# Optimization experiments

Measured on AMD Instinct MI355X. Metric: run time of the kernel, lower is better.

The kernel has to match this reference:

```python
import jax, jax.numpy as jnp
from jax import lax
import numpy as np

B, P, N = 4, 12000, 100   # batch, max_pillars, max_points_per_pillar
H, W = 108, 124           # pseudo-image size from forward()
DN = ('NCHW', 'HWIO', 'NCHW')


def _conv(x, k, b):
    y = lax.conv_general_dilated(x, k, (1, 1), 'SAME', dimension_numbers=DN)
    return y + b[None, :, None, None]


def _cbr(x, k, b, s, t):
    # Conv2d + folded BatchNorm2d (eval: per-channel scale/shift) + ReLU
    y = _conv(x, k, b)
    return jax.nn.relu(y * s[None, :, None, None] + t[None, :, None, None])


def _pool(x):
    return lax.reduce_window(x, -jnp.inf, lax.max, (1, 1, 2, 2), (1, 1, 2, 2), 'VALID')


def setup_inputs() -> dict:
    key = jax.random.key(0)
    ks = iter(jax.random.split(key, 64))
    d = {}
    d['pillars'] = jax.random.normal(next(ks), (B, P, N, 9), jnp.float32)

    def w(shape, scale=0.05):
        return jax.random.normal(next(ks), shape, jnp.float32) * scale

    d['w1'] = w((9, 64)); d['b1'] = w((64,))
    d['s1'] = 1.0 + w((64,)); d['t1'] = w((64,))
    d['w2'] = w((64, 64)); d['b2'] = w((64,))
    d['s2'] = 1.0 + w((64,)); d['t2'] = w((64,))
    chans = [(64, 64), (64, 64), (64, 128), (128, 128), (128, 256), (256, 256)]
    for i, (ci, co) in enumerate(chans, 1):
        d['ck%d' % i] = w((3, 3, ci, co)); d['cb%d' % i] = w((co,))
        d['cs%d' % i] = 1.0 + w((co,)); d['ct%d' % i] = w((co,))
    d['hk1'] = w((3, 3, 256, 256)); d['hb1'] = w((256,))
    d['hk2'] = w((1, 1, 256, 10)); d['hb2'] = w((10,))
    d['num_points'] = jax.random.randint(next(ks), (B, P), 0, 100, jnp.int32)
    return d


def reference(pillars, w1, b1, s1, t1, w2, b2, s2, t2,
              ck1, cb1, cs1, ct1, ck2, cb2, cs2, ct2,
              ck3, cb3, cs3, ct3, ck4, cb4, cs4, ct4,
              ck5, cb5, cs5, ct5, ck6, cb6, cs6, ct6,
              hk1, hb1, hk2, hb2, num_points):
    # pillar feature net: Linear+BN(folded)+ReLU x2, batched over all points  [B,P,N,9] -> [B,P,N,64]
    h = jax.nn.relu((pillars @ w1 + b1) * s1 + t1)
    h = jax.nn.relu((h @ w2 + b2) * s2 + t2)
    # masked segment-max over the variable-length point groups
    mask = jnp.arange(N)[None, None, :] < num_points[:, :, None]          # [B,P,N]
    neg = jnp.finfo(h.dtype).min
    feat = jnp.max(jnp.where(mask[..., None], h, neg), axis=2)            # [B,P,64]
    valid = num_points > 0
    feat = jnp.where(valid[..., None], feat, 0.0)
    cnt = jnp.maximum(jnp.sum(valid, axis=1), 1).astype(feat.dtype)       # [B]
    mean = jnp.sum(feat, axis=1) / cnt[:, None]                           # [B,64]
    # nearest-interpolate a 1x1 map to HxW == broadcast
    x = jnp.broadcast_to(mean[:, :, None, None], (pillars.shape[0], 64, H, W))
    # 2D backbone
    x = _cbr(x, ck1, cb1, cs1, ct1); x = _cbr(x, ck2, cb2, cs2, ct2); x = _pool(x)
    x = _cbr(x, ck3, cb3, cs3, ct3); x = _cbr(x, ck4, cb4, cs4, ct4); x = _pool(x)
    x = _cbr(x, ck5, cb5, cs5, ct5); x = _cbr(x, ck6, cb6, cs6, ct6)
    # detection head
    y = jax.nn.relu(_conv(x, hk1, hb1))
    return _conv(y, hk2, hb2)   # [B, num_classes+7=10, 27, 31]
```

## Files before the change

kernel.cpp:

```cpp
#include <hip/hip_runtime.h>

typedef __bf16 vbf8 __attribute__((ext_vector_type(8)));
typedef __bf16 vbf4 __attribute__((ext_vector_type(4)));
typedef unsigned short us8 __attribute__((ext_vector_type(8)));
typedef float f32x4 __attribute__((ext_vector_type(4)));
typedef float f32x4u __attribute__((ext_vector_type(4), aligned(4)));

#define NBLK 64

__device__ __forceinline__ int caseof(int h, int H, int e) {
  if (h < 0 || h >= H) return -1;
  if (h < e) return h;
  if (h >= H - e) return h - (H - 1) + 2 * e;
  return e;
}
__device__ __forceinline__ int repof(int i, int H, int eo) {
  return (i <= eo) ? i : H - 1 - 2 * eo + i;
}

__device__ __forceinline__ void gridbar(int* bar) {
  __syncthreads();
  if (threadIdx.x == 0) {
    int* cnt = bar; int* gen = bar + 1;
    int g = __hip_atomic_load(gen, __ATOMIC_RELAXED, __HIP_MEMORY_SCOPE_AGENT);
    if (__hip_atomic_fetch_add(cnt, 1, __ATOMIC_ACQ_REL, __HIP_MEMORY_SCOPE_AGENT) == NBLK - 1) {
      __hip_atomic_store(cnt, 0, __ATOMIC_RELAXED, __HIP_MEMORY_SCOPE_AGENT);
      __hip_atomic_store(gen, g + 1, __ATOMIC_RELEASE, __HIP_MEMORY_SCOPE_AGENT);
    } else {
      while (__hip_atomic_load(gen, __ATOMIC_RELAXED, __HIP_MEMORY_SCOPE_AGENT) == g)
        __builtin_amdgcn_s_sleep(8);
      __threadfence();
    }
  }
  __syncthreads();
}

__global__ void setup_kernel(const float* __restrict__ w1, const float* __restrict__ b1,
                             const float* __restrict__ s1, const float* __restrict__ t1,
                             const float* __restrict__ w2, const float* __restrict__ b2,
                             const float* __restrict__ s2, const float* __restrict__ t2,
                             __bf16* __restrict__ wfrag, float* __restrict__ be2f) {
  int l = threadIdx.x;
  int s = l & 15, g = l >> 4;
#pragma unroll
  for (int m = 0; m < 4; ++m) {
    int c = 32 * (m & 1) + 8 * (s >> 2) + 4 * (m >> 1) + (s & 3);
#pragma unroll
    for (int e = 0; e < 8; ++e) {
      int k = g * 8 + e;
      float v = 0.f;
      if (k < 9)       v = w1[k * 64 + c] * s1[c];
      else if (k == 9) v = fmaf(b1[c], s1[c], t1[c]);
      wfrag[(m * 64 + l) * 8 + e] = (__bf16)v;
    }
    int co = s + 16 * m;
#pragma unroll
    for (int e = 0; e < 8; ++e) {
      int k = g * 8 + e;
      wfrag[((4 + m) * 64 + l) * 8 + e] = (__bf16)(w2[k * 64 + co] * s2[co]);
      wfrag[((8 + m) * 64 + l) * 8 + e] = (__bf16)(w2[(32 + k) * 64 + co] * s2[co]);
    }
    be2f[m * 64 + l] = fmaf(b2[co], s2[co], t2[co]);
  }
}

__global__ __launch_bounds__(256) void convw_kernel(
    const float* __restrict__ k1, const float* __restrict__ k2,
    const float* __restrict__ k3, const float* __restrict__ k4,
    const float* __restrict__ k5, const float* __restrict__ k6,
    const float* __restrict__ kh, __bf16* __restrict__ wT) {
  __shared__ float tile[64][65];
  const int tCI[7]    = {64, 64, 64, 128, 128, 256, 256};
  const int tCO[7]    = {64, 64, 128, 128, 256, 256, 256};
  const int tOFF[7]   = {0, 36864, 73728, 147456, 294912, 589824, 1179648};
  const int tTILES[7] = {9, 9, 18, 36, 72, 144, 144};
  int bid = blockIdx.x;
  int ti = 0, acc = 0;
  while (ti < 6 && bid >= acc + tTILES[ti]) { acc += tTILES[ti]; ++ti; }
  int lt = bid - acc;
  int CI = tCI[ti], CO = tCO[ti];
  const float* src;
  if (ti == 0) src = k1; else if (ti == 1) src = k2; else if (ti == 2) src = k3;
  else if (ti == 3) src = k4; else if (ti == 4) src = k5; else if (ti == 5) src = k6;
  else src = kh;
  int cot = CO / 64, tpt = (CI / 64) * cot;
  int tap = lt / tpt; int r2 = lt - tap * tpt;
  int ci0 = (r2 / cot) * 64, co0 = (r2 % cot) * 64;
  const float* sp = src + (size_t)(tap * CI + ci0) * CO + co0;
  int t = threadIdx.x;
  int lr = t >> 6, lc = t & 63;
#pragma unroll
  for (int rr = 0; rr < 64; rr += 4)
    tile[rr + lr][lc] = sp[(size_t)(rr + lr) * CO + lc];
  __syncthreads();
  __bf16* dst = wT + tOFF[ti] + ((size_t)tap * CO + co0) * CI + ci0;
#pragma unroll
  for (int rr = 0; rr < 64; rr += 4)
    dst[(size_t)(rr + lr) * CI + lc] = (__bf16)tile[lc][rr + lr];
}

__global__ __launch_bounds__(256) void pillar_kernel(
    const float* __restrict__ pil, const int* __restrict__ npt,
    const __bf16* __restrict__ wfrag, const float* __restrict__ be2f,
    float* __restrict__ partial, int* __restrict__ pcnt)
{
  __shared__ float redf[4][64];
  __shared__ int redc[4];
  const int tid = threadIdx.x;
  const int wv = tid >> 6, lane = tid & 63;
  const int s = lane & 15, g = lane >> 4;
  const int wid = blockIdx.x * 4 + wv;
  const int b = wid / 6000;
  const int p0 = (wid - b * 6000) * 2;

  vbf8 w1f[4], w2f0[4], w2f1[4];
  float be2[4];
#pragma unroll
  for (int m = 0; m < 4; ++m) {
    w1f[m]  = *(const vbf8*)(wfrag + ((0 + m) * 64 + lane) * 8);
    w2f0[m] = *(const vbf8*)(wfrag + ((4 + m) * 64 + lane) * 8);
    w2f1[m] = *(const vbf8*)(wfrag + ((8 + m) * 64 + lane) * 8);
    be2[m] = be2f[m * 64 + lane];
  }

  float fsum[4] = {0.f, 0.f, 0.f, 0.f};
  int cnt = 0;

  for (int i = 0; i < 2; ++i) {
    int pidx = b * 12000 + p0 + i;
    int np = npt[pidx];
    if (np <= 0) continue;
    ++cnt;
    float feat[4][4];
#pragma unroll
    for (int n = 0; n < 4; ++n)
#pragma unroll
      for (int r = 0; r < 4; ++r) feat[n][r] = 0.f;

    int ngrp = (np + 15) >> 4;
    const float* pbase = pil + (size_t)pidx * 900;
    const float* pp0 = pbase + s * 9;
    f32x4u lo = *(const f32x4u*)pp0;
    f32x4u hi = *(const f32x4u*)(pp0 + 4);
    float v8 = pp0[8];
    for (int grp = 0; grp < ngrp; ++grp) {
      int g2 = min(grp + 1, ngrp - 1);
      int ptn = min(g2 * 16 + s, 99);
      const float* ppn = pbase + ptn * 9;
      f32x4u nlo = *(const f32x4u*)ppn;
      f32x4u nhi = *(const f32x4u*)(ppn + 4);
      float nv8 = ppn[8];

      vbf8 b1f;
      b1f[0] = (__bf16)(g == 0 ? lo[0] : (g == 1 ? v8 : 0.f));
      b1f[1] = (__bf16)(g == 0 ? lo[1] : (g == 1 ? 1.0f : 0.f));
      b1f[2] = (__bf16)(g == 0 ? lo[2] : 0.f);
      b1f[3] = (__bf16)(g == 0 ? lo[3] : 0.f);
      b1f[4] = (__bf16)(g == 0 ? hi[0] : 0.f);
      b1f[5] = (__bf16)(g == 0 ? hi[1] : 0.f);
      b1f[6] = (__bf16)(g == 0 ? hi[2] : 0.f);
      b1f[7] = (__bf16)(g == 0 ? hi[3] : 0.f);

      const f32x4 z = {0.f, 0.f, 0.f, 0.f};
      f32x4 d1[4];
#pragma unroll
      for (int m = 0; m < 4; ++m)
        d1[m] = __builtin_amdgcn_mfma_f32_16x16x32_bf16(w1f[m], b1f, z, 0, 0, 0);

      vbf8 a2f0, a2f1;
#pragma unroll
      for (int r = 0; r < 4; ++r) {
        a2f0[r]     = (__bf16)fmaxf(d1[0][r], 0.f);
        a2f1[r]     = (__bf16)fmaxf(d1[1][r], 0.f);
        a2f0[4 + r] = (__bf16)fmaxf(d1[2][r], 0.f);
        a2f1[4 + r] = (__bf16)fmaxf(d1[3][r], 0.f);
      }

      f32x4 d2[4];
#pragma unroll
      for (int n = 0; n < 4; ++n) {
        f32x4 cb = {be2[n], be2[n], be2[n], be2[n]};
        d2[n] = __builtin_amdgcn_mfma_f32_16x16x32_bf16(a2f0, w2f0[n], cb, 0, 0, 0);
        d2[n] = __builtin_amdgcn_mfma_f32_16x16x32_bf16(a2f1, w2f1[n], d2[n], 0, 0, 0);
      }
      if (((grp + 1) << 4) <= np) {
#pragma unroll
        for (int n = 0; n < 4; ++n)
#pragma unroll
          for (int r = 0; r < 4; ++r) feat[n][r] = fmaxf(feat[n][r], d2[n][r]);
      } else {
#pragma unroll
        for (int n = 0; n < 4; ++n)
#pragma unroll
          for (int r = 0; r < 4; ++r) {
            float vv = (grp * 16 + 4 * g + r < np) ? d2[n][r] : 0.f;
            feat[n][r] = fmaxf(feat[n][r], vv);
          }
      }
      lo = nlo; hi = nhi; v8 = nv8;
    }
#pragma unroll
    for (int n = 0; n < 4; ++n) {
      float m = fmaxf(fmaxf(feat[n][0], feat[n][1]), fmaxf(feat[n][2], feat[n][3]));
      m = fmaxf(m, __shfl_xor(m, 16));
      m = fmaxf(m, __shfl_xor(m, 32));
      fsum[n] += m;
    }
  }
  if (g == 0) {
#pragma unroll
    for (int n = 0; n < 4; ++n) redf[wv][s + 16 * n] = fsum[n];
  }
  if (lane == 0) redc[wv] = cnt;
  __syncthreads();
  if (tid < 64) {
    float tot = redf[0][tid] + redf[1][tid] + redf[2][tid] + redf[3][tid];
    partial[blockIdx.x * 64 + tid] = tot;
    if (tid == 0) pcnt[blockIdx.x] = redc[0] + redc[1] + redc[2] + redc[3];
  }
}

__global__ void mean_kernel(const float* __restrict__ partial,
                            const int* __restrict__ pcnt,
                            __bf16* __restrict__ x0,
                            __bf16* __restrict__ zbuf, int* __restrict__ bar) {
  int b = blockIdx.x, t = threadIdx.x;
  if (b == 0) {
    zbuf[t] = (__bf16)0.f;
    if (t < 2) bar[t] = 0;
  }
  int c = t & 63, q = t >> 6;
  float sum = 0.f;
  for (int w = q; w < 1500; w += 4) sum += partial[(b * 1500 + w) * 64 + c];
  int cl = 0;
  for (int w = t; w < 1500; w += 256) cl += pcnt[b * 1500 + w];
  __shared__ float sh[256];
  __shared__ int shc[256];
  sh[t] = sum; shc[t] = cl;
  __syncthreads();
  for (int o = 128; o > 0; o >>= 1) {
    if (t < o) shc[t] += shc[t + o];
    __syncthreads();
  }
  if (t < 64) {
    float tot = sh[t] + sh[t + 64] + sh[t + 128] + sh[t + 192];
    x0[b * 64 + t] = (__bf16)(tot / (float)(shc[0] > 0 ? shc[0] : 1));
  }
}

template <int CI, int CO, int H, int EIN, bool HAS_BN, bool OUT_F32>
__device__ __forceinline__ void caseconv_dev(
    int wid, const __bf16* __restrict__ xin, const __bf16* __restrict__ wt,
    const float* __restrict__ cb, const float* __restrict__ cs,
    const float* __restrict__ ct, __bf16* __restrict__ yout,
    float* __restrict__ yf32, const __bf16* __restrict__ zbuf)
{
  constexpr int EOUT = EIN + 1;
  constexpr int NBI = 2 * EIN + 1;
  constexpr int NBO = 2 * EOUT + 1;
  constexpr int M = NBO * NBO * 4;
  constexpr int NT = CO / 16;
  constexpr int KC = CI / 32;
  constexpr int MT = (M + 31) / 32;
  if (wid >= MT * NT) return;
  const int lane = threadIdx.x & 63;
  const int s = lane & 15, g = lane >> 4;
  const int nt = wid % NT, mt = wid / NT;

  const __bf16* pa[2][9];
#pragma unroll
  for (int mf = 0; mf < 2; ++mf) {
    int m = mt * 32 + mf * 16 + s; if (m >= M) m = M - 1;
    int b = m & 3, q = m >> 2;
    int bw = q % NBO, bh = q / NBO;
    int reph = repof(bh, H, EOUT), repw = repof(bw, H, EOUT);
#pragma unroll
    for (int dh = 0; dh < 3; ++dh)
#pragma unroll
      for (int dw = 0; dw < 3; ++dw) {
        int jh = caseof(reph + dh - 1, H, EIN);
        int jw = caseof(repw + dw - 1, H, EIN);
        bool v = (jh >= 0) && (jw >= 0);
        pa[mf][dh * 3 + dw] =
            v ? xin + (size_t)((jh * NBI + jw) * 4 + b) * CI : zbuf;
      }
  }

  f32x4 acc0 = {0.f, 0.f, 0.f, 0.f}, acc1 = {0.f, 0.f, 0.f, 0.f};
#pragma unroll
  for (int tap = 0; tap < 9; ++tap) {
    const __bf16* wtap = wt + ((size_t)tap * CO + nt * 16) * CI + 8 * g;
#pragma unroll
    for (int ck = 0; ck < KC; ++ck) {
      vbf8 a0 = *(const vbf8*)(pa[0][tap] + ck * 32 + 8 * g);
      vbf8 a1 = *(const vbf8*)(pa[1][tap] + ck * 32 + 8 * g);
      vbf8 bb = *(const vbf8*)(wtap + (size_t)s * CI + ck * 32);
      acc0 = __builtin_amdgcn_mfma_f32_16x16x32_bf16(a0, bb, acc0, 0, 0, 0);
      acc1 = __builtin_amdgcn_mfma_f32_16x16x32_bf16(a1, bb, acc1, 0, 0, 0);
    }
  }

  int co = nt * 16 + s;
  float sc, sh;
  if (HAS_BN) { sc = cs[co]; sh = fmaf(cb[co], sc, ct[co]); }
  else        { sc = 1.f;    sh = cb[co]; }
#pragma unroll
  for (int mf = 0; mf < 2; ++mf) {
    f32x4 acc = mf ? acc1 : acc0;
#pragma unroll
    for (int r = 0; r < 4; ++r) {
      int m = mt * 32 + mf * 16 + 4 * g + r;
      if (m < M) {
        float v = fmaxf(fmaf(acc[r], sc, sh), 0.f);
        if constexpr (OUT_F32) yf32[(size_t)m * CO + co] = v;
        else                   yout[(size_t)m * CO + co] = (__bf16)v;
      }
    }
  }
}

template <int C, int HOUT, int EIN>
__device__ __forceinline__ void casepool_dev(int gtid, const __bf16* __restrict__ xin,
                                             __bf16* __restrict__ yout) {
  constexpr int EOUT = (EIN + 1) / 2;
  constexpr int NBI = 2 * EIN + 1;
  constexpr int NBO = 2 * EOUT + 1;
  constexpr int C8 = C / 8;
  for (int idx = gtid; idx < NBO * NBO * 4 * C8; idx += NBLK * 256) {
    int c8 = idx % C8; int rest = idx / C8;
    int b = rest & 3; int pos = rest >> 2;
    int iw = pos % NBO, ih = pos / NBO;
    int rh = repof(ih, HOUT, EOUT), rw = repof(iw, HOUT, EOUT);
    int h0 = caseof(2 * rh, 2 * HOUT, EIN), h1 = caseof(2 * rh + 1, 2 * HOUT, EIN);
    int w0 = caseof(2 * rw, 2 * HOUT, EIN), w1 = caseof(2 * rw + 1, 2 * HOUT, EIN);
    const unsigned short* xp = (const unsigned short*)xin;
    us8 v00 = *(const us8*)(xp + (size_t)((h0 * NBI + w0) * 4 + b) * C + c8 * 8);
    us8 v01 = *(const us8*)(xp + (size_t)((h0 * NBI + w1) * 4 + b) * C + c8 * 8);
    us8 v10 = *(const us8*)(xp + (size_t)((h1 * NBI + w0) * 4 + b) * C + c8 * 8);
    us8 v11 = *(const us8*)(xp + (size_t)((h1 * NBI + w1) * 4 + b) * C + c8 * 8);
    us8 o;
#pragma unroll
    for (int e = 0; e < 8; ++e) {
      unsigned short a = v00[e] > v01[e] ? v00[e] : v01[e];
      unsigned short c = v10[e] > v11[e] ? v10[e] : v11[e];
      o[e] = a > c ? a : c;
    }
    *(us8*)((unsigned short*)yout + (size_t)((ih * NBO + iw) * 4 + b) * C + c8 * 8) = o;
  }
}

__device__ __forceinline__ void head2c_dev(int gtid, const float* __restrict__ x,
                                           const float* __restrict__ wk,
                                           const float* __restrict__ bias,
                                           float* __restrict__ y) {
  for (int idx = gtid; idx < 121 * 4 * 16; idx += NBLK * 256) {
    int co = idx & 15;
    if (co >= 10) continue;
    int q = idx >> 4;
    const float* xr = x + (size_t)q * 256;
    float acc = 0.f;
#pragma unroll 4
    for (int ci = 0; ci < 256; ci += 4) {
      float4 in4 = *(const float4*)(xr + ci);
      acc = fmaf(in4.x, wk[(ci + 0) * 10 + co], acc);
      acc = fmaf(in4.y, wk[(ci + 1) * 10 + co], acc);
      acc = fmaf(in4.z, wk[(ci + 2) * 10 + co], acc);
      acc = fmaf(in4.w, wk[(ci + 3) * 10 + co], acc);
    }
    y[(size_t)q * 10 + co] = acc + bias[co];
  }
}

__device__ __forceinline__ void scatter_dev(int gtid, const float* __restrict__ y,
                                            float* __restrict__ out) {
  for (int idx = gtid; idx < 4 * 10 * 27 * 31; idx += NBLK * 256) {
    int c = idx % 31;
    int r = (idx / 31) % 27;
    int ch = (idx / (31 * 27)) % 10;
    int b = idx / (31 * 27 * 10);
    int rr = (r <= 7) ? r : ((r >= 20) ? r - 11 : 7);
    int cc = (c <= 7) ? c : ((c >= 24) ? c - 15 : 7);
    int ph = caseof(rr, 16, 5), pw = caseof(cc, 16, 5);
    out[idx] = y[(size_t)(((ph * 11 + pw) * 4 + b)) * 10 + ch];
  }
}

__global__ __launch_bounds__(256) void backbone_kernel(
    const __bf16* __restrict__ X0, __bf16* __restrict__ X1, __bf16* __restrict__ X2,
    __bf16* __restrict__ P1, __bf16* __restrict__ X3, __bf16* __restrict__ X4,
    __bf16* __restrict__ P2, __bf16* __restrict__ X5, __bf16* __restrict__ X6,
    float* __restrict__ XH, float* __restrict__ h2out,
    const __bf16* wt1, const __bf16* wt2, const __bf16* wt3, const __bf16* wt4,
    const __bf16* wt5, const __bf16* wt6, const __bf16* wth,
    const float* cb1, const float* cs1, const float* ct1,
    const float* cb2, const float* cs2, const float* ct2,
    const float* cb3, const float* cs3, const float* ct3,
    const float* cb4, const float* cs4, const float* ct4,
    const float* cb5, const float* cs5, const float* ct5,
    const float* cb6, const float* cs6, const float* ct6,
    const float* hb1, const float* hk2, const float* hb2,
    const __bf16* __restrict__ zbuf, int* __restrict__ bar, float* __restrict__ out)
{
  const int wid = blockIdx.x * 4 + (threadIdx.x >> 6);
  const int gtid = blockIdx.x * 256 + threadIdx.x;

  caseconv_dev<64, 64, 64, 0, true, false>(wid, X0, wt1, cb1, cs1, ct1, X1, nullptr, zbuf);
  gridbar(bar);
  caseconv_dev<64, 64, 64, 1, true, false>(wid, X1, wt2, cb2, cs2, ct2, X2, nullptr, zbuf);
  gridbar(bar);
  casepool_dev<64, 32, 2>(gtid, X2, P1);
  gridbar(bar);
  caseconv_dev<64, 128, 32, 1, true, false>(wid, P1, wt3, cb3, cs3, ct3, X3, nullptr, zbuf);
  gridbar(bar);
  caseconv_dev<128, 128, 32, 2, true, false>(wid, X3, wt4, cb4, cs4, ct4, X4, nullptr, zbuf);
  gridbar(bar);
  casepool_dev<128, 16, 3>(gtid, X4, P2);
  gridbar(bar);
  caseconv_dev<128, 256, 16, 2, true, false>(wid, P2, wt5, cb5, cs5, ct5, X5, nullptr, zbuf);
  gridbar(bar);
  caseconv_dev<256, 256, 16, 3, true, false>(wid, X5, wt6, cb6, cs6, ct6, X6, nullptr, zbuf);
  gridbar(bar);
  caseconv_dev<256, 256, 16, 4, false, true>(wid, X6, wth, hb1, nullptr, nullptr, nullptr, XH, zbuf);
  gridbar(bar);
  head2c_dev(gtid, XH, hk2, hb2, h2out);
  gridbar(bar);
  scatter_dev(gtid, h2out, out);
}

extern "C" void kernel_launch(void* const* d_in, const int* in_sizes, int n_in,
                              void* d_out, int out_size, void* d_ws, size_t ws_size,
                              hipStream_t stream) {
  (void)in_sizes; (void)n_in; (void)out_size; (void)ws_size;
  const float* pillars = (const float*)d_in[0];
  const float* w1 = (const float*)d_in[1];
  const float* b1 = (const float*)d_in[2];
  const float* s1 = (const float*)d_in[3];
  const float* t1 = (const float*)d_in[4];
  const float* w2 = (const float*)d_in[5];
  const float* b2 = (const float*)d_in[6];
  const float* s2 = (const float*)d_in[7];
  const float* t2 = (const float*)d_in[8];
  const float* ck[6], *cbv[6], *csv[6], *ctv[6];
  for (int i = 0; i < 6; ++i) {
    ck[i]  = (const float*)d_in[9 + i * 4];
    cbv[i] = (const float*)d_in[10 + i * 4];
    csv[i] = (const float*)d_in[11 + i * 4];
    ctv[i] = (const float*)d_in[12 + i * 4];
  }
  const float* hk1 = (const float*)d_in[33];
  const float* hb1 = (const float*)d_in[34];
  const float* hk2 = (const float*)d_in[35];
  const float* hb2 = (const float*)d_in[36];
  const int* num_points = (const int*)d_in[37];
  float* out = (float*)d_out;

  char* wsb = (char*)d_ws;
  size_t off = 0;
  auto alloc = [&](size_t n) { char* p = wsb + off; off = (off + n + 255) & ~(size_t)255; return p; };
  float*  ppart = (float*)alloc(1536000);
  int*    pcnt  = (int*)alloc(24000);
  __bf16* wfrag = (__bf16*)alloc(12288);
  float*  be2f  = (float*)alloc(1024);
  __bf16* wT    = (__bf16*)alloc(3538944);
  __bf16* zbuf  = (__bf16*)alloc(512);
  int*    bar   = (int*)alloc(256);
  __bf16* X0    = (__bf16*)alloc(512);
  __bf16* X1    = (__bf16*)alloc(4608);
  __bf16* X2    = (__bf16*)alloc(12800);
  __bf16* P1    = (__bf16*)alloc(4608);
  __bf16* X3    = (__bf16*)alloc(25600);
  __bf16* X4    = (__bf16*)alloc(50176);
  __bf16* P2    = (__bf16*)alloc(25600);
  __bf16* X5    = (__bf16*)alloc(100352);
  __bf16* X6    = (__bf16*)alloc(165888);
  float*  XH    = (float*)alloc(495616);
  float*  h2out = (float*)alloc(19360);

  __bf16* wt1 = wT + 0;       __bf16* wt2 = wT + 36864;
  __bf16* wt3 = wT + 73728;   __bf16* wt4 = wT + 147456;
  __bf16* wt5 = wT + 294912;  __bf16* wt6 = wT + 589824;
  __bf16* wth = wT + 1179648;

  setup_kernel<<<1, 64, 0, stream>>>(w1, b1, s1, t1, w2, b2, s2, t2, wfrag, be2f);
  convw_kernel<<<432, 256, 0, stream>>>(ck[0], ck[1], ck[2], ck[3], ck[4], ck[5],
                                        hk1, wT);
  pillar_kernel<<<6000, 256, 0, stream>>>(pillars, num_points, wfrag, be2f,
                                          ppart, pcnt);
  mean_kernel<<<4, 256, 0, stream>>>(ppart, pcnt, X0, zbuf, bar);
  backbone_kernel<<<NBLK, 256, 0, stream>>>(
      X0, X1, X2, P1, X3, X4, P2, X5, X6, XH, h2out,
      wt1, wt2, wt3, wt4, wt5, wt6, wth,
      cbv[0], csv[0], ctv[0], cbv[1], csv[1], ctv[1],
      cbv[2], csv[2], ctv[2], cbv[3], csv[3], ctv[3],
      cbv[4], csv[4], ctv[4], cbv[5], csv[5], ctv[5],
      hb1, hk2, hb2, zbuf, bar, out);
}
```

Measured before the change: 332.6 us.

## Fuse max-pools into following convs and head 1x1 conv into scatter

Each 2x2 max-pool is now computed on the fly inside the next convolution's A-operand loads, taking the max of four bf16 vectors. This removes the separate pool stages, their buffers and two grid barriers. The 1x1 head conv is fused with the output scatter, which drops another barrier, and the grid barrier is reworked to use atomic RMW polling with an acquire fence. The trade-off is redundant pooling work (each pooled value is recomputed per tap and per N-tile) and redundant 1x1 dot products for replicated output pixels.

```diff
diff --git a/kernel.cpp b/kernel.cpp
--- a/kernel.cpp
+++ b/kernel.cpp
@@ -1,7 +1,6 @@
 #include <hip/hip_runtime.h>
 
 typedef __bf16 vbf8 __attribute__((ext_vector_type(8)));
-typedef __bf16 vbf4 __attribute__((ext_vector_type(4)));
 typedef unsigned short us8 __attribute__((ext_vector_type(8)));
 typedef float f32x4 __attribute__((ext_vector_type(4)));
 typedef float f32x4u __attribute__((ext_vector_type(4), aligned(4)));
@@ -18,21 +17,29 @@
   return (i <= eo) ? i : H - 1 - 2 * eo + i;
 }
 
+__device__ __forceinline__ vbf8 max8(vbf8 a, vbf8 b) {
+  us8 ua = __builtin_bit_cast(us8, a), ub = __builtin_bit_cast(us8, b);
+  us8 o;
+#pragma unroll
+  for (int e = 0; e < 8; ++e) o[e] = ua[e] > ub[e] ? ua[e] : ub[e];
+  return __builtin_bit_cast(vbf8, o);
+}
+
 __device__ __forceinline__ void gridbar(int* bar) {
   __syncthreads();
   if (threadIdx.x == 0) {
     int* cnt = bar; int* gen = bar + 1;
-    int g = __hip_atomic_load(gen, __ATOMIC_RELAXED, __HIP_MEMORY_SCOPE_AGENT);
+    int g = __hip_atomic_fetch_add(gen, 0, __ATOMIC_RELAXED, __HIP_MEMORY_SCOPE_AGENT);
     if (__hip_atomic_fetch_add(cnt, 1, __ATOMIC_ACQ_REL, __HIP_MEMORY_SCOPE_AGENT) == NBLK - 1) {
-      __hip_atomic_store(cnt, 0, __ATOMIC_RELAXED, __HIP_MEMORY_SCOPE_AGENT);
-      __hip_atomic_store(gen, g + 1, __ATOMIC_RELEASE, __HIP_MEMORY_SCOPE_AGENT);
+      __hip_atomic_fetch_add(cnt, -NBLK, __ATOMIC_RELAXED, __HIP_MEMORY_SCOPE_AGENT);
+      __hip_atomic_fetch_add(gen, 1, __ATOMIC_RELEASE, __HIP_MEMORY_SCOPE_AGENT);
     } else {
-      while (__hip_atomic_load(gen, __ATOMIC_RELAXED, __HIP_MEMORY_SCOPE_AGENT) == g)
-        __builtin_amdgcn_s_sleep(8);
-      __threadfence();
+      while (__hip_atomic_fetch_add(gen, 0, __ATOMIC_RELAXED, __HIP_MEMORY_SCOPE_AGENT) == g)
+        __builtin_amdgcn_s_sleep(32);
     }
   }
   __syncthreads();
+  __builtin_amdgcn_fence(__ATOMIC_ACQUIRE, "agent");
 }
 
 __global__ void setup_kernel(const float* __restrict__ w1, const float* __restrict__ b1,
@@ -248,52 +255,78 @@
   }
 }
 
-template <int CI, int CO, int H, int EIN, bool HAS_BN, bool OUT_F32>
+template <int CI, int CO, int H, int EIN, bool POOL, bool HAS_BN, bool OUT_F32>
 __device__ __forceinline__ void caseconv_dev(
     int wid, const __bf16* __restrict__ xin, const __bf16* __restrict__ wt,
     const float* __restrict__ cb, const float* __restrict__ cs,
     const float* __restrict__ ct, __bf16* __restrict__ yout,
     float* __restrict__ yf32, const __bf16* __restrict__ zbuf)
 {
-  constexpr int EOUT = EIN + 1;
-  constexpr int NBI = 2 * EIN + 1;
-  constexpr int NBO = 2 * EOUT + 1;
-  constexpr int M = NBO * NBO * 4;
-  constexpr int NT = CO / 16;
-  constexpr int KC = CI / 32;
-  constexpr int MT = (M + 31) / 32;
+  constexpr int EV   = POOL ? (EIN + 1) / 2 : EIN;
+  constexpr int EOUT = EV + 1;
+  constexpr int NBI  = 2 * EIN + 1;
+  constexpr int HX   = POOL ? 2 * H : H;
+  constexpr int NBO  = 2 * EOUT + 1;
+  constexpr int M    = NBO * NBO * 4;
+  constexpr int NT   = CO / 16;
+  constexpr int KC   = CI / 32;
+  constexpr int MT   = (M + 31) / 32;
   if (wid >= MT * NT) return;
   const int lane = threadIdx.x & 63;
   const int s = lane & 15, g = lane >> 4;
   const int nt = wid % NT, mt = wid / NT;
 
-  const __bf16* pa[2][9];
+  int reph[2], repw[2], bsel[2];
 #pragma unroll
   for (int mf = 0; mf < 2; ++mf) {
     int m = mt * 32 + mf * 16 + s; if (m >= M) m = M - 1;
-    int b = m & 3, q = m >> 2;
+    bsel[mf] = m & 3; int q = m >> 2;
     int bw = q % NBO, bh = q / NBO;
-    int reph = repof(bh, H, EOUT), repw = repof(bw, H, EOUT);
-#pragma unroll
-    for (int dh = 0; dh < 3; ++dh)
-#pragma unroll
-      for (int dw = 0; dw < 3; ++dw) {
-        int jh = caseof(reph + dh - 1, H, EIN);
-        int jw = caseof(repw + dw - 1, H, EIN);
+    reph[mf] = repof(bh, H, EOUT); repw[mf] = repof(bw, H, EOUT);
+  }
+
+  f32x4 acc0 = {0.f, 0.f, 0.f, 0.f}, acc1 = {0.f, 0.f, 0.f, 0.f};
+#pragma unroll
+  for (int tap = 0; tap < 9; ++tap) {
+    const int dh = tap / 3, dw = tap % 3;
+    const __bf16* wtap = wt + ((size_t)tap * CO + nt * 16) * CI + 8 * g;
+    const __bf16* base[2][POOL ? 4 : 1];
+#pragma unroll
+    for (int mf = 0; mf < 2; ++mf) {
+      int vh = reph[mf] + dh - 1, vw = repw[mf] + dw - 1;
+      if constexpr (POOL) {
+        bool valid = (vh >= 0) && (vh < H) && (vw >= 0) && (vw < H);
+        int h0 = 0, h1 = 0, w0 = 0, w1 = 0;
+        if (valid) {
+          h0 = caseof(2 * vh, HX, EIN); h1 = caseof(2 * vh + 1, HX, EIN);
+          w0 = caseof(2 * vw, HX, EIN); w1 = caseof(2 * vw + 1, HX, EIN);
+        }
+        base[mf][0] = valid ? xin + (size_t)((h0 * NBI + w0) * 4 + bsel[mf]) * CI : zbuf;
+        base[mf][1] = valid ? xin + (size_t)((h0 * NBI + w1) * 4 + bsel[mf]) * CI : zbuf;
+        base[mf][2] = valid ? xin + (size_t)((h1 * NBI + w0) * 4 + bsel[mf]) * CI : zbuf;
+        base[mf][3] = valid ? xin + (size_t)((h1 * NBI + w1) * 4 + bsel[mf]) * CI : zbuf;
+      } else {
+        int jh = caseof(vh, H, EIN), jw = caseof(vw, H, EIN);
         bool v = (jh >= 0) && (jw >= 0);
-        pa[mf][dh * 3 + dw] =
-            v ? xin + (size_t)((jh * NBI + jw) * 4 + b) * CI : zbuf;
-      }
-  }
-
-  f32x4 acc0 = {0.f, 0.f, 0.f, 0.f}, acc1 = {0.f, 0.f, 0.f, 0.f};
-#pragma unroll
-  for (int tap = 0; tap < 9; ++tap) {
-    const __bf16* wtap = wt + ((size_t)tap * CO + nt * 16) * CI + 8 * g;
+        base[mf][0] = v ? xin + (size_t)((jh * NBI + jw) * 4 + bsel[mf]) * CI : zbuf;
+      }
+    }
 #pragma unroll
     for (int ck = 0; ck < KC; ++ck) {
-      vbf8 a0 = *(const vbf8*)(pa[0][tap] + ck * 32 + 8 * g);
-      vbf8 a1 = *(const vbf8*)(pa[1][tap] + ck * 32 + 8 * g);
+      vbf8 a0, a1;
+      if constexpr (POOL) {
+        a0 = max8(max8(*(const vbf8*)(base[0][0] + ck * 32 + 8 * g),
+                       *(const vbf8*)(base[0][1] + ck * 32 + 8 * g)),
+                  max8(*(const vbf8*)(base[0][2] + ck * 32 + 8 * g),
+                       *(const vbf8*)(base[0][3] + ck * 32 + 8 * g)));
+        a1 = max8(max8(*(const vbf8*)(base[1][0] + ck * 32 + 8 * g),
+                       *(const vbf8*)(base[1][1] + ck * 32 + 8 * g)),
+                  max8(*(const vbf8*)(base[1][2] + ck * 32 + 8 * g),
+                       *(const vbf8*)(base[1][3] + ck * 32 + 8 * g)));
+      } else {
+        a0 = *(const vbf8*)(base[0][0] + ck * 32 + 8 * g);
+        a1 = *(const vbf8*)(base[1][0] + ck * 32 + 8 * g);
+      }
       vbf8 bb = *(const vbf8*)(wtap + (size_t)s * CI + ck * 32);
       acc0 = __builtin_amdgcn_mfma_f32_16x16x32_bf16(a0, bb, acc0, 0, 0, 0);
       acc1 = __builtin_amdgcn_mfma_f32_16x16x32_bf16(a1, bb, acc1, 0, 0, 0);
@@ -319,60 +352,10 @@
   }
 }
 
-template <int C, int HOUT, int EIN>
-__device__ __forceinline__ void casepool_dev(int gtid, const __bf16* __restrict__ xin,
-                                             __bf16* __restrict__ yout) {
-  constexpr int EOUT = (EIN + 1) / 2;
-  constexpr int NBI = 2 * EIN + 1;
-  constexpr int NBO = 2 * EOUT + 1;
-  constexpr int C8 = C / 8;
-  for (int idx = gtid; idx < NBO * NBO * 4 * C8; idx += NBLK * 256) {
-    int c8 = idx % C8; int rest = idx / C8;
-    int b = rest & 3; int pos = rest >> 2;
-    int iw = pos % NBO, ih = pos / NBO;
-    int rh = repof(ih, HOUT, EOUT), rw = repof(iw, HOUT, EOUT);
-    int h0 = caseof(2 * rh, 2 * HOUT, EIN), h1 = caseof(2 * rh + 1, 2 * HOUT, EIN);
-    int w0 = caseof(2 * rw, 2 * HOUT, EIN), w1 = caseof(2 * rw + 1, 2 * HOUT, EIN);
-    const unsigned short* xp = (const unsigned short*)xin;
-    us8 v00 = *(const us8*)(xp + (size_t)((h0 * NBI + w0) * 4 + b) * C + c8 * 8);
-    us8 v01 = *(const us8*)(xp + (size_t)((h0 * NBI + w1) * 4 + b) * C + c8 * 8);
-    us8 v10 = *(const us8*)(xp + (size_t)((h1 * NBI + w0) * 4 + b) * C + c8 * 8);
-    us8 v11 = *(const us8*)(xp + (size_t)((h1 * NBI + w1) * 4 + b) * C + c8 * 8);
-    us8 o;
-#pragma unroll
-    for (int e = 0; e < 8; ++e) {
-      unsigned short a = v00[e] > v01[e] ? v00[e] : v01[e];
-      unsigned short c = v10[e] > v11[e] ? v10[e] : v11[e];
-      o[e] = a > c ? a : c;
-    }
-    *(us8*)((unsigned short*)yout + (size_t)((ih * NBO + iw) * 4 + b) * C + c8 * 8) = o;
-  }
-}
-
-__device__ __forceinline__ void head2c_dev(int gtid, const float* __restrict__ x,
-                                           const float* __restrict__ wk,
-                                           const float* __restrict__ bias,
-                                           float* __restrict__ y) {
-  for (int idx = gtid; idx < 121 * 4 * 16; idx += NBLK * 256) {
-    int co = idx & 15;
-    if (co >= 10) continue;
-    int q = idx >> 4;
-    const float* xr = x + (size_t)q * 256;
-    float acc = 0.f;
-#pragma unroll 4
-    for (int ci = 0; ci < 256; ci += 4) {
-      float4 in4 = *(const float4*)(xr + ci);
-      acc = fmaf(in4.x, wk[(ci + 0) * 10 + co], acc);
-      acc = fmaf(in4.y, wk[(ci + 1) * 10 + co], acc);
-      acc = fmaf(in4.z, wk[(ci + 2) * 10 + co], acc);
-      acc = fmaf(in4.w, wk[(ci + 3) * 10 + co], acc);
-    }
-    y[(size_t)q * 10 + co] = acc + bias[co];
-  }
-}
-
-__device__ __forceinline__ void scatter_dev(int gtid, const float* __restrict__ y,
-                                            float* __restrict__ out) {
+__device__ __forceinline__ void headscatter_dev(int gtid, const float* __restrict__ x,
+                                                const float* __restrict__ wk,
+                                                const float* __restrict__ bias,
+                                                float* __restrict__ out) {
   for (int idx = gtid; idx < 4 * 10 * 27 * 31; idx += NBLK * 256) {
     int c = idx % 31;
     int r = (idx / 31) % 27;
@@ -381,15 +364,24 @@
     int rr = (r <= 7) ? r : ((r >= 20) ? r - 11 : 7);
     int cc = (c <= 7) ? c : ((c >= 24) ? c - 15 : 7);
     int ph = caseof(rr, 16, 5), pw = caseof(cc, 16, 5);
-    out[idx] = y[(size_t)(((ph * 11 + pw) * 4 + b)) * 10 + ch];
+    const float* xr = x + (size_t)((ph * 11 + pw) * 4 + b) * 256;
+    float a0 = 0.f, a1 = 0.f, a2 = 0.f, a3 = 0.f;
+#pragma unroll 4
+    for (int ci = 0; ci < 256; ci += 4) {
+      float4 in4 = *(const float4*)(xr + ci);
+      a0 = fmaf(in4.x, wk[(ci + 0) * 10 + ch], a0);
+      a1 = fmaf(in4.y, wk[(ci + 1) * 10 + ch], a1);
+      a2 = fmaf(in4.z, wk[(ci + 2) * 10 + ch], a2);
+      a3 = fmaf(in4.w, wk[(ci + 3) * 10 + ch], a3);
+    }
+    out[idx] = (a0 + a1) + (a2 + a3) + bias[ch];
   }
 }
 
 __global__ __launch_bounds__(256) void backbone_kernel(
     const __bf16* __restrict__ X0, __bf16* __restrict__ X1, __bf16* __restrict__ X2,
-    __bf16* __restrict__ P1, __bf16* __restrict__ X3, __bf16* __restrict__ X4,
-    __bf16* __restrict__ P2, __bf16* __restrict__ X5, __bf16* __restrict__ X6,
-    float* __restrict__ XH, float* __restrict__ h2out,
+    __bf16* __restrict__ X3, __bf16* __restrict__ X4, __bf16* __restrict__ X5,
+    __bf16* __restrict__ X6, float* __restrict__ XH,
     const __bf16* wt1, const __bf16* wt2, const __bf16* wt3, const __bf16* wt4,
     const __bf16* wt5, const __bf16* wt6, const __bf16* wth,
     const float* cb1, const float* cs1, const float* ct1,
@@ -404,27 +396,21 @@
   const int wid = blockIdx.x * 4 + (threadIdx.x >> 6);
   const int gtid = blockIdx.x * 256 + threadIdx.x;
 
-  caseconv_dev<64, 64, 64, 0, true, false>(wid, X0, wt1, cb1, cs1, ct1, X1, nullptr, zbuf);
-  gridbar(bar);
-  caseconv_dev<64, 64, 64, 1, true, false>(wid, X1, wt2, cb2, cs2, ct2, X2, nullptr, zbuf);
-  gridbar(bar);
-  casepool_dev<64, 32, 2>(gtid, X2, P1);
-  gridbar(bar);
-  caseconv_dev<64, 128, 32, 1, true, false>(wid, P1, wt3, cb3, cs3, ct3, X3, nullptr, zbuf);
-  gridbar(bar);
-  caseconv_dev<128, 128, 32, 2, true, false>(wid, X3, wt4, cb4, cs4, ct4, X4, nullptr, zbuf);
-  gridbar(bar);
-  casepool_dev<128, 16, 3>(gtid, X4, P2);
-  gridbar(bar);
-  caseconv_dev<128, 256, 16, 2, true, false>(wid, P2, wt5, cb5, cs5, ct5, X5, nullptr, zbuf);
-  gridbar(bar);
-  caseconv_dev<256, 256, 16, 3, true, false>(wid, X5, wt6, cb6, cs6, ct6, X6, nullptr, zbuf);
-  gridbar(bar);
-  caseconv_dev<256, 256, 16, 4, false, true>(wid, X6, wth, hb1, nullptr, nullptr, nullptr, XH, zbuf);
-  gridbar(bar);
-  head2c_dev(gtid, XH, hk2, hb2, h2out);
-  gridbar(bar);
-  scatter_dev(gtid, h2out, out);
+  caseconv_dev<64, 64, 64, 0, false, true, false>(wid, X0, wt1, cb1, cs1, ct1, X1, nullptr, zbuf);
+  gridbar(bar);
+  caseconv_dev<64, 64, 64, 1, false, true, false>(wid, X1, wt2, cb2, cs2, ct2, X2, nullptr, zbuf);
+  gridbar(bar);
+  caseconv_dev<64, 128, 32, 2, true, true, false>(wid, X2, wt3, cb3, cs3, ct3, X3, nullptr, zbuf);
+  gridbar(bar);
+  caseconv_dev<128, 128, 32, 2, false, true, false>(wid, X3, wt4, cb4, cs4, ct4, X4, nullptr, zbuf);
+  gridbar(bar);
+  caseconv_dev<128, 256, 16, 3, true, true, false>(wid, X4, wt5, cb5, cs5, ct5, X5, nullptr, zbuf);
+  gridbar(bar);
+  caseconv_dev<256, 256, 16, 3, false, true, false>(wid, X5, wt6, cb6, cs6, ct6, X6, nullptr, zbuf);
+  gridbar(bar);
+  caseconv_dev<256, 256, 16, 4, false, false, true>(wid, X6, wth, hb1, nullptr, nullptr, nullptr, XH, zbuf);
+  gridbar(bar);
+  headscatter_dev(gtid, XH, hk2, hb2, out);
 }
 
 extern "C" void kernel_launch(void* const* d_in, const int* in_sizes, int n_in,
@@ -467,14 +453,11 @@
   __bf16* X0    = (__bf16*)alloc(512);
   __bf16* X1    = (__bf16*)alloc(4608);
   __bf16* X2    = (__bf16*)alloc(12800);
-  __bf16* P1    = (__bf16*)alloc(4608);
   __bf16* X3    = (__bf16*)alloc(25600);
   __bf16* X4    = (__bf16*)alloc(50176);
-  __bf16* P2    = (__bf16*)alloc(25600);
   __bf16* X5    = (__bf16*)alloc(100352);
   __bf16* X6    = (__bf16*)alloc(165888);
   float*  XH    = (float*)alloc(495616);
-  float*  h2out = (float*)alloc(19360);
 
   __bf16* wt1 = wT + 0;       __bf16* wt2 = wT + 36864;
   __bf16* wt3 = wT + 73728;   __bf16* wt4 = wT + 147456;
@@ -488,7 +471,7 @@
                                           ppart, pcnt);
   mean_kernel<<<4, 256, 0, stream>>>(ppart, pcnt, X0, zbuf, bar);
   backbone_kernel<<<NBLK, 256, 0, stream>>>(
-      X0, X1, X2, P1, X3, X4, P2, X5, X6, XH, h2out,
+      X0, X1, X2, X3, X4, X5, X6, XH,
       wt1, wt2, wt3, wt4, wt5, wt6, wth,
       cbv[0], csv[0], ctv[0], cbv[1], csv[1], ctv[1],
       cbv[2], csv[2], ctv[2], cbv[3], csv[3], ctv[3],
```

New measurement: 390.5 us. 17.4% more time.
